# Performance work log

Hardware: AMD Instinct MI355X
Metric: run time of the kernel (lower is better)

## Reference

```python
import jax, jax.numpy as jnp
import numpy as np

D_MODEL = 1024
NUM_HEADS = 16
HEAD_DIM = D_MODEL // NUM_HEADS
SCALE = HEAD_DIM ** -0.5


def setup_inputs() -> dict:
    key = jax.random.key(0)
    k1, k2, k3 = jax.random.split(key, 3)
    B, N = 2, 2048
    x = jax.random.normal(k1, (B, N, D_MODEL), dtype=jnp.float32)
    w_qkv = jax.random.normal(k2, (D_MODEL, 3 * D_MODEL), dtype=jnp.float32) * (D_MODEL ** -0.5)
    b_qkv = jnp.zeros((3 * D_MODEL,), dtype=jnp.float32)
    w_proj = jax.random.normal(k3, (D_MODEL, D_MODEL), dtype=jnp.float32) * (D_MODEL ** -0.5)
    b_proj = jnp.zeros((D_MODEL,), dtype=jnp.float32)
    return {"x": x, "w_qkv": w_qkv, "b_qkv": b_qkv, "w_proj": w_proj, "b_proj": b_proj}


def reference(x, w_qkv, b_qkv, w_proj, b_proj):
    B, N, C = x.shape
    H, Hd = NUM_HEADS, HEAD_DIM
    # fused QKV projection: [B,N,3C] -> [3,B,H,N,Hd]
    qkv = (x @ w_qkv + b_qkv).reshape(B, N, 3, H, Hd).transpose(2, 0, 3, 1, 4)
    q, k, v = qkv[0], qkv[1], qkv[2]
    # manual scaled dot-product attention (full NxN scores, as in source)
    attn = jnp.einsum('bhqd,bhkd->bhqk', q, k) * SCALE
    attn = jax.nn.softmax(attn, axis=-1)
    out = jnp.einsum('bhqk,bhkd->bhqd', attn, v)  # [B,H,N,Hd]
    out = out.transpose(0, 2, 1, 3).reshape(B, N, C)
    return out @ w_proj + b_proj
```

## Files before the change

kernel.cpp:

```cpp
#include <hip/hip_runtime.h>
#include <hip/hip_bf16.h>
#include <stdint.h>

typedef __attribute__((ext_vector_type(8))) __bf16 bf16x8;
typedef __attribute__((ext_vector_type(4))) __bf16 bf16x4;
typedef __attribute__((ext_vector_type(4))) float f32x4;

#define AS1 __attribute__((address_space(1)))
#define AS3 __attribute__((address_space(3)))

__device__ __forceinline__ void load_lds16(const void* g, void* l) {
    __builtin_amdgcn_global_load_lds((const AS1 void*)g, (AS3 void*)l, 16, 0, 0);
}

__device__ __forceinline__ float m3(float a, float b, float c) {
    return fmaxf(fmaxf(a, b), c);
}

constexpr float QSCALE = 0.18033688011112042f;

__device__ __forceinline__ int sigma32(int kv) {
    return (kv < 16) ? ((kv >> 2) * 8 + (kv & 3))
                     : (((kv - 16) >> 2) * 8 + 4 + ((kv - 16) & 3));
}

__device__ __forceinline__ void tconv_body(const float* __restrict__ src,
                                           __bf16* __restrict__ dst,
                                           int R, int C, int c0, int r0, int t) {
    __shared__ float tile[32][33];
    const int tx = t & 31, ty = t >> 5;
    #pragma unroll
    for (int i = 0; i < 32; i += 8)
        tile[ty + i][tx] = src[(size_t)(r0 + ty + i) * C + c0 + tx];
    __syncthreads();
    #pragma unroll
    for (int i = 0; i < 32; i += 8)
        dst[(size_t)(c0 + ty + i) * R + r0 + tx] = (__bf16)tile[tx][ty + i];
}

__global__ __launch_bounds__(256)
void prep(const float* __restrict__ x, const float* __restrict__ w_qkv,
          const float* __restrict__ w_proj, __bf16* __restrict__ x_bf,
          __bf16* __restrict__ wqkvT, __bf16* __restrict__ wprojT) {
    const int bid = blockIdx.x;
    const int t = threadIdx.x;
    if (bid < 1024) {
        const float4* xv = (const float4*)x;
        bf16x4* ov = (bf16x4*)x_bf;
        int i = bid * 256 + t;
        #pragma unroll
        for (int it = 0; it < 4; ++it, i += 262144) {
            float4 v = xv[i];
            bf16x4 r;
            r[0] = (__bf16)v.x; r[1] = (__bf16)v.y;
            r[2] = (__bf16)v.z; r[3] = (__bf16)v.w;
            ov[i] = r;
        }
    } else if (bid < 1024 + 3072) {
        const int b = bid - 1024;
        tconv_body(w_qkv, wqkvT, 1024, 3072, (b % 96) * 32, (b / 96) * 32, t);
    } else {
        const int b = bid - 4096;
        tconv_body(w_proj, wprojT, 1024, 1024, (b & 31) * 32, (b >> 5) * 32, t);
    }
}

template <int MODE>
__global__ __launch_bounds__(256)
void gemm128(const __bf16* __restrict__ A, const __bf16* __restrict__ Bt,
             const float* __restrict__ bias, void* __restrict__ outp,
             int M, int Nn, int K) {
    __shared__ __bf16 As[3][128][32];
    __shared__ __bf16 Bs[3][128][32];
    const int t = threadIdx.x;
    const int w = t >> 6, l = t & 63;
    const int lrow = l & 15, lhi = l >> 4;
    const int wr = (w >> 1) * 64, wc = (w & 1) * 64;

    int m0, n0;
    {
        const int f = blockIdx.x + blockIdx.y * gridDim.x;
        if ((gridDim.y & 3) == 0 && (gridDim.x & 1) == 0) {
            const int c = f & 7, i = f >> 3;
            const int nch = gridDim.x >> 1;
            const int mrow = i / nch, ncol = i % nch;
            m0 = ((c & 3) * (gridDim.y >> 2) + mrow) * 128;
            n0 = ((c >> 2) * nch + ncol) * 128;
        } else {
            m0 = blockIdx.y * 128; n0 = blockIdx.x * 128;
        }
    }

    f32x4 acc[4][4] = {};

    const int sr = t >> 2;
    const int dc = (t & 3) * 8;
    const int scsw = ((t & 3) ^ ((sr >> 1) & 3)) * 8;
    const __bf16* agb = A + (size_t)(m0 + sr) * K + scsw;
    const __bf16* bgb = Bt + (size_t)(n0 + sr) * K + scsw;

#define STAGE_G(BUF, KT)                                                   \
    { load_lds16(agb + (KT), &As[BUF][sr][dc]);                            \
      load_lds16(agb + (size_t)64 * K + (KT), &As[BUF][64 + sr][dc]);      \
      load_lds16(bgb + (KT), &Bs[BUF][sr][dc]);                            \
      load_lds16(bgb + (size_t)64 * K + (KT), &Bs[BUF][64 + sr][dc]); }

    STAGE_G(0, 0)
    STAGE_G(1, 32)

    const int rofs = (lhi ^ ((lrow >> 1) & 3)) << 4;
    const int nt = K >> 5;
    int cur = 0, pre = 2;
    for (int tt = 0; tt < nt; ++tt) {
        if (tt + 2 < nt) {
            STAGE_G(pre, (tt + 2) * 32)
            asm volatile("s_waitcnt vmcnt(8)" ::: "memory");
        } else if (tt + 1 < nt) {
            asm volatile("s_waitcnt vmcnt(4)" ::: "memory");
        } else {
            asm volatile("s_waitcnt vmcnt(0)" ::: "memory");
        }
        __builtin_amdgcn_sched_barrier(0);
        __builtin_amdgcn_s_barrier();
        __builtin_amdgcn_sched_barrier(0);

        bf16x8 af[4], bfv[4];
        #pragma unroll
        for (int i = 0; i < 4; ++i)
            af[i] = *(const bf16x8*)((const char*)&As[cur][wr + i * 16 + lrow][0] + rofs);
        #pragma unroll
        for (int j = 0; j < 4; ++j)
            bfv[j] = *(const bf16x8*)((const char*)&Bs[cur][wc + j * 16 + lrow][0] + rofs);
        __builtin_amdgcn_s_setprio(1);
        #pragma unroll
        for (int i = 0; i < 4; ++i)
            #pragma unroll
            for (int j = 0; j < 4; ++j)
                acc[i][j] = __builtin_amdgcn_mfma_f32_16x16x32_bf16(
                    af[i], bfv[j], acc[i][j], 0, 0, 0);
        __builtin_amdgcn_s_setprio(0);

        __builtin_amdgcn_sched_barrier(0);
        asm volatile("s_waitcnt lgkmcnt(0)" ::: "memory");
        __builtin_amdgcn_s_barrier();
        __builtin_amdgcn_sched_barrier(0);

        cur = (cur == 2) ? 0 : cur + 1;
        pre = (pre == 2) ? 0 : pre + 1;
    }
#undef STAGE_G

    #pragma unroll
    for (int i = 0; i < 4; ++i)
        #pragma unroll
        for (int j = 0; j < 4; ++j)
            #pragma unroll
            for (int r = 0; r < 4; ++r) {
                int row = m0 + wr + i * 16 + lhi * 4 + r;
                int col = n0 + wc + j * 16 + lrow;
                float val = acc[i][j][r] + bias[col];
                if (MODE == 0) {
                    int which = col >> 10;
                    int h = (col >> 6) & 15;
                    int d = col & 63;
                    int b = row >> 11;
                    int n = row & 2047;
                    int bh = (b << 4) + h;
                    if (which == 2) {
                        ((__bf16*)outp)[(size_t)2 * (32 * 2048 * 64) +
                                        ((size_t)bh * 64 + d) * 2048 +
                                        (n & ~31) + sigma32(n & 31)] = (__bf16)val;
                    } else {
                        if (which == 0) val *= QSCALE;
                        ((__bf16*)outp)[(size_t)which * (32 * 2048 * 64) +
                                        ((size_t)bh * 2048 + n) * 64 + d] = (__bf16)val;
                    }
                } else {
                    ((float*)outp)[(size_t)row * Nn + col] = val;
                }
            }
}

__global__ __launch_bounds__(256)
void attn_fwd(const __bf16* __restrict__ q, const __bf16* __restrict__ k,
              const __bf16* __restrict__ vt, __bf16* __restrict__ out) {
    __shared__ __bf16 KsV[2][2][64][64];
    __shared__ __bf16 VsV[2][2][64][64];
    char* ksB = (char*)KsV;
    char* vsB = (char*)VsV;

    const int t = threadIdx.x;
    const int w = t >> 6, l = t & 63;
    const int lrow = l & 15, lhi = l >> 4;
    const int bh = blockIdx.y;
    const int q0 = blockIdx.x * 128 + w * 32;

    const __bf16* qp = q + ((size_t)bh * 2048 + q0) * 64;
    bf16x8 qfA0 = *(const bf16x8*)(qp + lrow * 64 + lhi * 8);
    bf16x8 qfA1 = *(const bf16x8*)(qp + lrow * 64 + 32 + lhi * 8);
    bf16x8 qfB0 = *(const bf16x8*)(qp + (16 + lrow) * 64 + lhi * 8);
    bf16x8 qfB1 = *(const bf16x8*)(qp + (16 + lrow) * 64 + 32 + lhi * 8);

    f32x4 oA[4] = {}, oB[4] = {};
    float mA = -1e30f, mB = -1e30f;
    float lA = 0.f, lB = 0.f;

    const __bf16* kg = k + (size_t)bh * 2048 * 64;
    const __bf16* vg = vt + (size_t)bh * 64 * 2048;

    const int sr = t >> 3;
    const int sw8 = ((t & 7) ^ (sr & 7)) * 8;
    const int rsw = (lrow & 7) << 4;

    {
        char* kd = ksB + t * 16;
        char* vd = vsB + t * 16;
        load_lds16(kg + (size_t)sr * 64 + sw8, kd);
        load_lds16(kg + (size_t)(32 + sr) * 64 + sw8, kd + 4096);
        load_lds16(kg + (size_t)(64 + sr) * 64 + sw8, kd + 8192);
        load_lds16(kg + (size_t)(96 + sr) * 64 + sw8, kd + 12288);
        load_lds16(vg + (size_t)sr * 2048 + sw8, vd);
        load_lds16(vg + (size_t)(32 + sr) * 2048 + sw8, vd + 4096);
        load_lds16(vg + (size_t)sr * 2048 + 64 + sw8, vd + 8192);
        load_lds16(vg + (size_t)(32 + sr) * 2048 + 64 + sw8, vd + 12288);
    }

    const __bf16* kst = kg + (size_t)(128 + sr) * 64 + sw8;
    const __bf16* vst = vg + (size_t)sr * 2048 + 128 + sw8;

    int cur = 0;
    for (int kv0 = 0; kv0 < 2048; kv0 += 128) {
        __syncthreads();
        if (kv0 + 128 < 2048) {
            char* kd = ksB + (cur ^ 1) * 16384 + t * 16;
            char* vd = vsB + (cur ^ 1) * 16384 + t * 16;
            load_lds16(kst, kd);
            load_lds16(kst + 32 * 64, kd + 4096);
            load_lds16(kst + 64 * 64, kd + 8192);
            load_lds16(kst + 96 * 64, kd + 12288);
            load_lds16(vst, vd);
            load_lds16(vst + 32 * 2048, vd + 4096);
            load_lds16(vst + 64, vd + 8192);
            load_lds16(vst + 32 * 2048 + 64, vd + 12288);
            kst += 8192; vst += 128;
        }
        #pragma unroll
        for (int h = 0; h < 2; ++h) {
            const char* kb = ksB + cur * 16384 + h * 8192 + lrow * 128;
            const char* vb = vsB + cur * 16384 + h * 8192 + lrow * 128;
            const int o0 = (lhi << 4) ^ rsw;
            const int o4 = ((4 + lhi) << 4) ^ rsw;

            f32x4 sA0 = {}, sA1 = {}, sA2 = {}, sA3 = {};
            f32x4 sB0 = {}, sB1 = {}, sB2 = {}, sB3 = {};
            __builtin_amdgcn_s_setprio(1);
            {
                bf16x8 kf0, kf1;
#define QK_GROUP(SA, SB, BASE)                                                 \
                kf0 = *(const bf16x8*)(kb + (BASE) + o0);                      \
                kf1 = *(const bf16x8*)(kb + (BASE) + o4);                      \
                SA = __builtin_amdgcn_mfma_f32_16x16x32_bf16(kf0, qfA0, SA, 0, 0, 0); \
                SA = __builtin_amdgcn_mfma_f32_16x16x32_bf16(kf1, qfA1, SA, 0, 0, 0); \
                SB = __builtin_amdgcn_mfma_f32_16x16x32_bf16(kf0, qfB0, SB, 0, 0, 0); \
                SB = __builtin_amdgcn_mfma_f32_16x16x32_bf16(kf1, qfB1, SB, 0, 0, 0);
                QK_GROUP(sA0, sB0, 0)
                QK_GROUP(sA1, sB1, 2048)
                QK_GROUP(sA2, sB2, 4096)
                QK_GROUP(sA3, sB3, 6144)
#undef QK_GROUP
            }
            __builtin_amdgcn_s_setprio(0);

            float u0 = m3(sA0[0], sA0[1], sA0[2]);
            float u1 = m3(sA0[3], sA1[0], sA1[1]);
            float u2 = m3(sA1[2], sA1[3], sA2[0]);
            float u3 = m3(sA2[1], sA2[2], sA2[3]);
            float u4 = m3(sA3[0], sA3[1], sA3[2]);
            float tmA = fmaxf(m3(u0, u1, u2), m3(u3, u4, sA3[3]));
            float v0 = m3(sB0[0], sB0[1], sB0[2]);
            float v1 = m3(sB0[3], sB1[0], sB1[1]);
            float v2 = m3(sB1[2], sB1[3], sB2[0]);
            float v3 = m3(sB2[1], sB2[2], sB2[3]);
            float v4 = m3(sB3[0], sB3[1], sB3[2]);
            float tmB = fmaxf(m3(v0, v1, v2), m3(v3, v4, sB3[3]));
            tmA = fmaxf(tmA, __shfl_xor(tmA, 16, 64));
            tmA = fmaxf(tmA, __shfl_xor(tmA, 32, 64));
            tmB = fmaxf(tmB, __shfl_xor(tmB, 16, 64));
            tmB = fmaxf(tmB, __shfl_xor(tmB, 32, 64));
            if (!__all(tmA <= mA + 8.0f && tmB <= mB + 8.0f)) {
                float mnA = fmaxf(mA, tmA), mnB = fmaxf(mB, tmB);
                float cA = __builtin_amdgcn_exp2f(mA - mnA);
                float cB = __builtin_amdgcn_exp2f(mB - mnB);
                lA *= cA; lB *= cB;
                #pragma unroll
                for (int dt = 0; dt < 4; ++dt)
                    #pragma unroll
                    for (int r = 0; r < 4; ++r) { oA[dt][r] *= cA; oB[dt][r] *= cB; }
                mA = mnA; mB = mnB;
            }
            float pA[16], pB[16];
            #pragma unroll
            for (int r = 0; r < 4; ++r) {
                pA[r]      = __builtin_amdgcn_exp2f(sA0[r] - mA);
                pA[4 + r]  = __builtin_amdgcn_exp2f(sA1[r] - mA);
                pA[8 + r]  = __builtin_amdgcn_exp2f(sA2[r] - mA);
                pA[12 + r] = __builtin_amdgcn_exp2f(sA3[r] - mA);
                pB[r]      = __builtin_amdgcn_exp2f(sB0[r] - mB);
                pB[4 + r]  = __builtin_amdgcn_exp2f(sB1[r] - mB);
                pB[8 + r]  = __builtin_amdgcn_exp2f(sB2[r] - mB);
                pB[12 + r] = __builtin_amdgcn_exp2f(sB3[r] - mB);
            }
            float rsA = 0.f, rsB = 0.f;
            #pragma unroll
            for (int j = 0; j < 16; ++j) { rsA += pA[j]; rsB += pB[j]; }
            lA += rsA; lB += rsB;

            bf16x8 pfA0, pfA1, pfB0, pfB1;
            #pragma unroll
            for (int j = 0; j < 8; ++j) {
                pfA0[j] = (__bf16)pA[j]; pfA1[j] = (__bf16)pA[8 + j];
                pfB0[j] = (__bf16)pB[j]; pfB1[j] = (__bf16)pB[8 + j];
            }

            __builtin_amdgcn_s_setprio(1);
            #pragma unroll
            for (int dt = 0; dt < 4; ++dt) {
                bf16x8 vf0 = *(const bf16x8*)(vb + dt * 2048 + o0);
                bf16x8 vf1 = *(const bf16x8*)(vb + dt * 2048 + o4);
                oA[dt] = __builtin_amdgcn_mfma_f32_16x16x32_bf16(vf0, pfA0, oA[dt], 0, 0, 0);
                oA[dt] = __builtin_amdgcn_mfma_f32_16x16x32_bf16(vf1, pfA1, oA[dt], 0, 0, 0);
                oB[dt] = __builtin_amdgcn_mfma_f32_16x16x32_bf16(vf0, pfB0, oB[dt], 0, 0, 0);
                oB[dt] = __builtin_amdgcn_mfma_f32_16x16x32_bf16(vf1, pfB1, oB[dt], 0, 0, 0);
            }
            __builtin_amdgcn_s_setprio(0);
        }
        cur ^= 1;
    }

    lA += __shfl_xor(lA, 16, 64); lA += __shfl_xor(lA, 32, 64);
    lB += __shfl_xor(lB, 16, 64); lB += __shfl_xor(lB, 32, 64);
    float invA = __builtin_amdgcn_rcpf(lA);
    float invB = __builtin_amdgcn_rcpf(lB);

    const int b = bh >> 4, h = bh & 15;
    __bf16* orowA = out + ((size_t)(b * 2048 + q0 + lrow)) * 1024 + h * 64;
    __bf16* orowB = out + ((size_t)(b * 2048 + q0 + 16 + lrow)) * 1024 + h * 64;
    #pragma unroll
    for (int dt = 0; dt < 4; ++dt) {
        bf16x4 ovA, ovB;
        #pragma unroll
        for (int r = 0; r < 4; ++r) {
            ovA[r] = (__bf16)(oA[dt][r] * invA);
            ovB[r] = (__bf16)(oB[dt][r] * invB);
        }
        *(bf16x4*)(orowA + dt * 16 + lhi * 4) = ovA;
        *(bf16x4*)(orowB + dt * 16 + lhi * 4) = ovB;
    }
}

extern "C" void kernel_launch(void* const* d_in, const int* in_sizes, int n_in,
                              void* d_out, int out_size, void* d_ws, size_t ws_size,
                              hipStream_t stream) {
    const float* x      = (const float*)d_in[0];
    const float* w_qkv  = (const float*)d_in[1];
    const float* b_qkv  = (const float*)d_in[2];
    const float* w_proj = (const float*)d_in[3];
    const float* b_proj = (const float*)d_in[4];
    float* out = (float*)d_out;

    __bf16* ws     = (__bf16*)d_ws;
    __bf16* x_bf   = ws;
    __bf16* wqkvT  = x_bf + 4096 * 1024;
    __bf16* wprojT = wqkvT + 3072 * 1024;
    __bf16* qb     = wprojT + 1024 * 1024;
    __bf16* kb     = qb + 32 * 2048 * 64;
    __bf16* vtb    = kb + 32 * 2048 * 64;
    __bf16* attn   = vtb + 32 * 2048 * 64;

    prep<<<5120, 256, 0, stream>>>(x, w_qkv, w_proj, x_bf, wqkvT, wprojT);
    gemm128<0><<<dim3(24, 32), 256, 0, stream>>>(x_bf, wqkvT, b_qkv, qb, 4096, 3072, 1024);
    attn_fwd<<<dim3(16, 32), 256, 0, stream>>>(qb, kb, vtb, attn);
    gemm128<1><<<dim3(8, 32), 256, 0, stream>>>(attn, wprojT, b_proj, out, 4096, 1024, 1024);
}
```

Measured before the change: 204.6 us.

## Software-pipeline attention: overlap next tile's QK MFMAs with current softmax/PV

Restructures the flash-attention inner loop into 64-key tiles with a triple-buffered LDS ring. The QK^T MFMAs for tile t+1 are issued before the softmax and PV of tile t, so matrix work can overlap the exp/max VALU work. This doubles the score register sets and shrinks the per-stage tile, which raises register pressure and adds more barriers.

```diff
diff --git a/kernel.cpp b/kernel.cpp
--- a/kernel.cpp
+++ b/kernel.cpp
@@ -184,8 +184,8 @@
 __global__ __launch_bounds__(256)
 void attn_fwd(const __bf16* __restrict__ q, const __bf16* __restrict__ k,
               const __bf16* __restrict__ vt, __bf16* __restrict__ out) {
-    __shared__ __bf16 KsV[2][2][64][64];
-    __shared__ __bf16 VsV[2][2][64][64];
+    __shared__ __bf16 KsV[3][64][64];
+    __shared__ __bf16 VsV[3][64][64];
     char* ksB = (char*)KsV;
     char* vsB = (char*)VsV;
 
@@ -211,131 +211,155 @@
     const int sr = t >> 3;
     const int sw8 = ((t & 7) ^ (sr & 7)) * 8;
     const int rsw = (lrow & 7) << 4;
+    const int t16 = t * 16;
 
     {
-        char* kd = ksB + t * 16;
-        char* vd = vsB + t * 16;
+        char* kd = ksB + t16;
+        char* vd = vsB + t16;
         load_lds16(kg + (size_t)sr * 64 + sw8, kd);
         load_lds16(kg + (size_t)(32 + sr) * 64 + sw8, kd + 4096);
-        load_lds16(kg + (size_t)(64 + sr) * 64 + sw8, kd + 8192);
-        load_lds16(kg + (size_t)(96 + sr) * 64 + sw8, kd + 12288);
         load_lds16(vg + (size_t)sr * 2048 + sw8, vd);
         load_lds16(vg + (size_t)(32 + sr) * 2048 + sw8, vd + 4096);
-        load_lds16(vg + (size_t)sr * 2048 + 64 + sw8, vd + 8192);
-        load_lds16(vg + (size_t)(32 + sr) * 2048 + 64 + sw8, vd + 12288);
-    }
-
-    const __bf16* kst = kg + (size_t)(128 + sr) * 64 + sw8;
-    const __bf16* vst = vg + (size_t)sr * 2048 + 128 + sw8;
-
-    int cur = 0;
-    for (int kv0 = 0; kv0 < 2048; kv0 += 128) {
+    }
+
+    const __bf16* kst  = kg + (size_t)(64 + sr) * 64 + sw8;
+    const __bf16* kst2 = kst + 32 * 64;
+    const __bf16* vst  = vg + (size_t)sr * 2048 + 64 + sw8;
+    const __bf16* vst2 = vst + 32 * 2048;
+
+    const int o0 = (lhi << 4) ^ rsw;
+    const int o4 = ((4 + lhi) << 4) ^ rsw;
+
+#define STAGE(DB)                                                              \
+    { char* kd = ksB + (DB) * 8192 + t16;                                      \
+      char* vd = vsB + (DB) * 8192 + t16;                                      \
+      load_lds16(kst, kd);  load_lds16(kst2, kd + 4096);                       \
+      load_lds16(vst, vd);  load_lds16(vst2, vd + 4096);                       \
+      kst += 4096; kst2 += 4096; vst += 64; vst2 += 64; }
+
+#define QK_TILE(SA0, SA1, SA2, SA3, SB0, SB1, SB2, SB3, KBUF)                  \
+    { const char* kb = ksB + (KBUF) * 8192 + lrow * 128;                       \
+      SA0 = (f32x4){}; SA1 = (f32x4){}; SA2 = (f32x4){}; SA3 = (f32x4){};      \
+      SB0 = (f32x4){}; SB1 = (f32x4){}; SB2 = (f32x4){}; SB3 = (f32x4){};      \
+      bf16x8 kf0, kf1;                                                         \
+      __builtin_amdgcn_s_setprio(1);                                           \
+      kf0 = *(const bf16x8*)(kb + o0);                                         \
+      kf1 = *(const bf16x8*)(kb + o4);                                         \
+      SA0 = __builtin_amdgcn_mfma_f32_16x16x32_bf16(kf0, qfA0, SA0, 0, 0, 0);  \
+      SA0 = __builtin_amdgcn_mfma_f32_16x16x32_bf16(kf1, qfA1, SA0, 0, 0, 0);  \
+      SB0 = __builtin_amdgcn_mfma_f32_16x16x32_bf16(kf0, qfB0, SB0, 0, 0, 0);  \
+      SB0 = __builtin_amdgcn_mfma_f32_16x16x32_bf16(kf1, qfB1, SB0, 0, 0, 0);  \
+      kf0 = *(const bf16x8*)(kb + 2048 + o0);                                  \
+      kf1 = *(const bf16x8*)(kb + 2048 + o4);                                  \
+      SA1 = __builtin_amdgcn_mfma_f32_16x16x32_bf16(kf0, qfA0, SA1, 0, 0, 0);  \
+      SA1 = __builtin_amdgcn_mfma_f32_16x16x32_bf16(kf1, qfA1, SA1, 0, 0, 0);  \
+      SB1 = __builtin_amdgcn_mfma_f32_16x16x32_bf16(kf0, qfB0, SB1, 0, 0, 0);  \
+      SB1 = __builtin_amdgcn_mfma_f32_16x16x32_bf16(kf1, qfB1, SB1, 0, 0, 0);  \
+      kf0 = *(const bf16x8*)(kb + 4096 + o0);                                  \
+      kf1 = *(const bf16x8*)(kb + 4096 + o4);                                  \
+      SA2 = __builtin_amdgcn_mfma_f32_16x16x32_bf16(kf0, qfA0, SA2, 0, 0, 0);  \
+      SA2 = __builtin_amdgcn_mfma_f32_16x16x32_bf16(kf1, qfA1, SA2, 0, 0, 0);  \
+      SB2 = __builtin_amdgcn_mfma_f32_16x16x32_bf16(kf0, qfB0, SB2, 0, 0, 0);  \
+      SB2 = __builtin_amdgcn_mfma_f32_16x16x32_bf16(kf1, qfB1, SB2, 0, 0, 0);  \
+      kf0 = *(const bf16x8*)(kb + 6144 + o0);                                  \
+      kf1 = *(const bf16x8*)(kb + 6144 + o4);                                  \
+      SA3 = __builtin_amdgcn_mfma_f32_16x16x32_bf16(kf0, qfA0, SA3, 0, 0, 0);  \
+      SA3 = __builtin_amdgcn_mfma_f32_16x16x32_bf16(kf1, qfA1, SA3, 0, 0, 0);  \
+      SB3 = __builtin_amdgcn_mfma_f32_16x16x32_bf16(kf0, qfB0, SB3, 0, 0, 0);  \
+      SB3 = __builtin_amdgcn_mfma_f32_16x16x32_bf16(kf1, qfB1, SB3, 0, 0, 0);  \
+      __builtin_amdgcn_s_setprio(0); }
+
+#define SM_PV(SA0, SA1, SA2, SA3, SB0, SB1, SB2, SB3, VBUF)                    \
+    { const char* vb = vsB + (VBUF) * 8192 + lrow * 128;                       \
+      float u0 = m3(SA0[0], SA0[1], SA0[2]);                                   \
+      float u1 = m3(SA0[3], SA1[0], SA1[1]);                                   \
+      float u2 = m3(SA1[2], SA1[3], SA2[0]);                                   \
+      float u3 = m3(SA2[1], SA2[2], SA2[3]);                                   \
+      float u4 = m3(SA3[0], SA3[1], SA3[2]);                                   \
+      float tmA = fmaxf(m3(u0, u1, u2), m3(u3, u4, SA3[3]));                   \
+      float v0 = m3(SB0[0], SB0[1], SB0[2]);                                   \
+      float v1 = m3(SB0[3], SB1[0], SB1[1]);                                   \
+      float v2 = m3(SB1[2], SB1[3], SB2[0]);                                   \
+      float v3 = m3(SB2[1], SB2[2], SB2[3]);                                   \
+      float v4 = m3(SB3[0], SB3[1], SB3[2]);                                   \
+      float tmB = fmaxf(m3(v0, v1, v2), m3(v3, v4, SB3[3]));                   \
+      tmA = fmaxf(tmA, __shfl_xor(tmA, 16, 64));                               \
+      tmA = fmaxf(tmA, __shfl_xor(tmA, 32, 64));                               \
+      tmB = fmaxf(tmB, __shfl_xor(tmB, 16, 64));                               \
+      tmB = fmaxf(tmB, __shfl_xor(tmB, 32, 64));                               \
+      if (!__all(tmA <= mA + 8.0f && tmB <= mB + 8.0f)) {                      \
+          float mnA = fmaxf(mA, tmA), mnB = fmaxf(mB, tmB);                    \
+          float cA = __builtin_amdgcn_exp2f(mA - mnA);                         \
+          float cB = __builtin_amdgcn_exp2f(mB - mnB);                         \
+          lA *= cA; lB *= cB;                                                  \
+          _Pragma("unroll")                                                    \
+          for (int dt = 0; dt < 4; ++dt)                                       \
+              _Pragma("unroll")                                                \
+              for (int r = 0; r < 4; ++r) { oA[dt][r] *= cA; oB[dt][r] *= cB; }\
+          mA = mnA; mB = mnB;                                                  \
+      }                                                                        \
+      float pA[16], pB[16];                                                    \
+      _Pragma("unroll")                                                        \
+      for (int r = 0; r < 4; ++r) {                                            \
+          pA[r]      = __builtin_amdgcn_exp2f(SA0[r] - mA);                    \
+          pA[4 + r]  = __builtin_amdgcn_exp2f(SA1[r] - mA);                    \
+          pA[8 + r]  = __builtin_amdgcn_exp2f(SA2[r] - mA);                    \
+          pA[12 + r] = __builtin_amdgcn_exp2f(SA3[r] - mA);                    \
+          pB[r]      = __builtin_amdgcn_exp2f(SB0[r] - mB);                    \
+          pB[4 + r]  = __builtin_amdgcn_exp2f(SB1[r] - mB);                    \
+          pB[8 + r]  = __builtin_amdgcn_exp2f(SB2[r] - mB);                    \
+          pB[12 + r] = __builtin_amdgcn_exp2f(SB3[r] - mB);                    \
+      }                                                                        \
+      float rsA = 0.f, rsB = 0.f;                                              \
+      _Pragma("unroll")                                                        \
+      for (int j = 0; j < 16; ++j) { rsA += pA[j]; rsB += pB[j]; }             \
+      lA += rsA; lB += rsB;                                                    \
+      bf16x8 pfA0, pfA1, pfB0, pfB1;                                           \
+      _Pragma("unroll")                                                        \
+      for (int j = 0; j < 8; ++j) {                                            \
+          pfA0[j] = (__bf16)pA[j]; pfA1[j] = (__bf16)pA[8 + j];                \
+          pfB0[j] = (__bf16)pB[j]; pfB1[j] = (__bf16)pB[8 + j];                \
+      }                                                                        \
+      __builtin_amdgcn_s_setprio(1);                                           \
+      _Pragma("unroll")                                                        \
+      for (int dt = 0; dt < 4; ++dt) {                                         \
+          bf16x8 vf0 = *(const bf16x8*)(vb + dt * 2048 + o0);                  \
+          bf16x8 vf1 = *(const bf16x8*)(vb + dt * 2048 + o4);                  \
+          oA[dt] = __builtin_amdgcn_mfma_f32_16x16x32_bf16(vf0, pfA0, oA[dt], 0, 0, 0); \
+          oA[dt] = __builtin_amdgcn_mfma_f32_16x16x32_bf16(vf1, pfA1, oA[dt], 0, 0, 0); \
+          oB[dt] = __builtin_amdgcn_mfma_f32_16x16x32_bf16(vf0, pfB0, oB[dt], 0, 0, 0); \
+          oB[dt] = __builtin_amdgcn_mfma_f32_16x16x32_bf16(vf1, pfB1, oB[dt], 0, 0, 0); \
+      }                                                                        \
+      __builtin_amdgcn_s_setprio(0); }
+
+    f32x4 xA0, xA1, xA2, xA3, xB0, xB1, xB2, xB3;
+    f32x4 yA0, yA1, yA2, yA3, yB0, yB1, yB2, yB3;
+
+    __syncthreads();
+    STAGE(1)
+    QK_TILE(xA0, xA1, xA2, xA3, xB0, xB1, xB2, xB3, 0)
+
+    for (int tt = 1; tt < 31; tt += 2) {
+        const int a = tt % 3;
+        const int b = (tt + 1) % 3;
+        const int c = (tt + 2) % 3;
         __syncthreads();
-        if (kv0 + 128 < 2048) {
-            char* kd = ksB + (cur ^ 1) * 16384 + t * 16;
-            char* vd = vsB + (cur ^ 1) * 16384 + t * 16;
-            load_lds16(kst, kd);
-            load_lds16(kst + 32 * 64, kd + 4096);
-            load_lds16(kst + 64 * 64, kd + 8192);
-            load_lds16(kst + 96 * 64, kd + 12288);
-            load_lds16(vst, vd);
-            load_lds16(vst + 32 * 2048, vd + 4096);
-            load_lds16(vst + 64, vd + 8192);
-            load_lds16(vst + 32 * 2048 + 64, vd + 12288);
-            kst += 8192; vst += 128;
-        }
-        #pragma unroll
-        for (int h = 0; h < 2; ++h) {
-            const char* kb = ksB + cur * 16384 + h * 8192 + lrow * 128;
-            const char* vb = vsB + cur * 16384 + h * 8192 + lrow * 128;
-            const int o0 = (lhi << 4) ^ rsw;
-            const int o4 = ((4 + lhi) << 4) ^ rsw;
-
-            f32x4 sA0 = {}, sA1 = {}, sA2 = {}, sA3 = {};
-            f32x4 sB0 = {}, sB1 = {}, sB2 = {}, sB3 = {};
-            __builtin_amdgcn_s_setprio(1);
-            {
-                bf16x8 kf0, kf1;
-#define QK_GROUP(SA, SB, BASE)                                                 \
-                kf0 = *(const bf16x8*)(kb + (BASE) + o0);                      \
-                kf1 = *(const bf16x8*)(kb + (BASE) + o4);                      \
-                SA = __builtin_amdgcn_mfma_f32_16x16x32_bf16(kf0, qfA0, SA, 0, 0, 0); \
-                SA = __builtin_amdgcn_mfma_f32_16x16x32_bf16(kf1, qfA1, SA, 0, 0, 0); \
-                SB = __builtin_amdgcn_mfma_f32_16x16x32_bf16(kf0, qfB0, SB, 0, 0, 0); \
-                SB = __builtin_amdgcn_mfma_f32_16x16x32_bf16(kf1, qfB1, SB, 0, 0, 0);
-                QK_GROUP(sA0, sB0, 0)
-                QK_GROUP(sA1, sB1, 2048)
-                QK_GROUP(sA2, sB2, 4096)
-                QK_GROUP(sA3, sB3, 6144)
-#undef QK_GROUP
-            }
-            __builtin_amdgcn_s_setprio(0);
-
-            float u0 = m3(sA0[0], sA0[1], sA0[2]);
-            float u1 = m3(sA0[3], sA1[0], sA1[1]);
-            float u2 = m3(sA1[2], sA1[3], sA2[0]);
-            float u3 = m3(sA2[1], sA2[2], sA2[3]);
-            float u4 = m3(sA3[0], sA3[1], sA3[2]);
-            float tmA = fmaxf(m3(u0, u1, u2), m3(u3, u4, sA3[3]));
-            float v0 = m3(sB0[0], sB0[1], sB0[2]);
-            float v1 = m3(sB0[3], sB1[0], sB1[1]);
-            float v2 = m3(sB1[2], sB1[3], sB2[0]);
-            float v3 = m3(sB2[1], sB2[2], sB2[3]);
-            float v4 = m3(sB3[0], sB3[1], sB3[2]);
-            float tmB = fmaxf(m3(v0, v1, v2), m3(v3, v4, sB3[3]));
-            tmA = fmaxf(tmA, __shfl_xor(tmA, 16, 64));
-            tmA = fmaxf(tmA, __shfl_xor(tmA, 32, 64));
-            tmB = fmaxf(tmB, __shfl_xor(tmB, 16, 64));
-            tmB = fmaxf(tmB, __shfl_xor(tmB, 32, 64));
-            if (!__all(tmA <= mA + 8.0f && tmB <= mB + 8.0f)) {
-                float mnA = fmaxf(mA, tmA), mnB = fmaxf(mB, tmB);
-                float cA = __builtin_amdgcn_exp2f(mA - mnA);
-                float cB = __builtin_amdgcn_exp2f(mB - mnB);
-                lA *= cA; lB *= cB;
-                #pragma unroll
-                for (int dt = 0; dt < 4; ++dt)
-                    #pragma unroll
-                    for (int r = 0; r < 4; ++r) { oA[dt][r] *= cA; oB[dt][r] *= cB; }
-                mA = mnA; mB = mnB;
-            }
-            float pA[16], pB[16];
-            #pragma unroll
-            for (int r = 0; r < 4; ++r) {
-                pA[r]      = __builtin_amdgcn_exp2f(sA0[r] - mA);
-                pA[4 + r]  = __builtin_amdgcn_exp2f(sA1[r] - mA);
-                pA[8 + r]  = __builtin_amdgcn_exp2f(sA2[r] - mA);
-                pA[12 + r] = __builtin_amdgcn_exp2f(sA3[r] - mA);
-                pB[r]      = __builtin_amdgcn_exp2f(sB0[r] - mB);
-                pB[4 + r]  = __builtin_amdgcn_exp2f(sB1[r] - mB);
-                pB[8 + r]  = __builtin_amdgcn_exp2f(sB2[r] - mB);
-                pB[12 + r] = __builtin_amdgcn_exp2f(sB3[r] - mB);
-            }
-            float rsA = 0.f, rsB = 0.f;
-            #pragma unroll
-            for (int j = 0; j < 16; ++j) { rsA += pA[j]; rsB += pB[j]; }
-            lA += rsA; lB += rsB;
-
-            bf16x8 pfA0, pfA1, pfB0, pfB1;
-            #pragma unroll
-            for (int j = 0; j < 8; ++j) {
-                pfA0[j] = (__bf16)pA[j]; pfA1[j] = (__bf16)pA[8 + j];
-                pfB0[j] = (__bf16)pB[j]; pfB1[j] = (__bf16)pB[8 + j];
-            }
-
-            __builtin_amdgcn_s_setprio(1);
-            #pragma unroll
-            for (int dt = 0; dt < 4; ++dt) {
-                bf16x8 vf0 = *(const bf16x8*)(vb + dt * 2048 + o0);
-                bf16x8 vf1 = *(const bf16x8*)(vb + dt * 2048 + o4);
-                oA[dt] = __builtin_amdgcn_mfma_f32_16x16x32_bf16(vf0, pfA0, oA[dt], 0, 0, 0);
-                oA[dt] = __builtin_amdgcn_mfma_f32_16x16x32_bf16(vf1, pfA1, oA[dt], 0, 0, 0);
-                oB[dt] = __builtin_amdgcn_mfma_f32_16x16x32_bf16(vf0, pfB0, oB[dt], 0, 0, 0);
-                oB[dt] = __builtin_amdgcn_mfma_f32_16x16x32_bf16(vf1, pfB1, oB[dt], 0, 0, 0);
-            }
-            __builtin_amdgcn_s_setprio(0);
-        }
-        cur ^= 1;
-    }
+        STAGE(b)
+        QK_TILE(yA0, yA1, yA2, yA3, yB0, yB1, yB2, yB3, a)
+        SM_PV(xA0, xA1, xA2, xA3, xB0, xB1, xB2, xB3, c)
+        __syncthreads();
+        STAGE(c)
+        QK_TILE(xA0, xA1, xA2, xA3, xB0, xB1, xB2, xB3, b)
+        SM_PV(yA0, yA1, yA2, yA3, yB0, yB1, yB2, yB3, a)
+    }
+    __syncthreads();
+    QK_TILE(yA0, yA1, yA2, yA3, yB0, yB1, yB2, yB3, 1)
+    SM_PV(xA0, xA1, xA2, xA3, xB0, xB1, xB2, xB3, 0)
+    SM_PV(yA0, yA1, yA2, yA3, yB0, yB1, yB2, yB3, 1)
+
+#undef STAGE
+#undef QK_TILE
+#undef SM_PV
 
     lA += __shfl_xor(lA, 16, 64); lA += __shfl_xor(lA, 32, 64);
     lB += __shfl_xor(lB, 16, 64); lB += __shfl_xor(lB, 32, 64);
```

Result: slower. 209.1 us (+2.2%).
